# Performance work log

Hardware: AMD Instinct MI355X
Metric: run time of the kernel (lower is better)

Reference implementation:

```python
import jax, jax.numpy as jnp
import numpy as np

EPS = 1e-5
N_HEADS = 16
TOP_K = 2


def _ln(x, g, b):
    m = x.mean(-1, keepdims=True)
    v = ((x - m) ** 2).mean(-1, keepdims=True)
    return (x - m) / jnp.sqrt(v + EPS) * g + b


def _block_fwd(x, ln1_g, ln1_b, ln2_g, ln2_b, Wq, bq, Wk, bk, Wv, bv, Wo, bo,
               Wr, br, e_w1, e_b1, e_w2, e_b2):
    B, S, D = x.shape
    H = N_HEADS
    hd = D // H
    # --- LN + causal MHA + residual (dropout is identity at eval) ---
    h = _ln(x, ln1_g, ln1_b)
    q = (h @ Wq + bq).reshape(B, S, H, hd).transpose(0, 2, 1, 3)  # [B,H,S,hd]
    k = (h @ Wk + bk).reshape(B, S, H, hd).transpose(0, 2, 1, 3)
    v = (h @ Wv + bv).reshape(B, S, H, hd).transpose(0, 2, 1, 3)
    scores = jnp.einsum('bhqd,bhkd->bhqk', q, k) / (hd ** 0.5)
    causal = jnp.tril(jnp.ones((S, S), dtype=bool))
    scores = jnp.where(causal, scores, -jnp.inf)
    attn = jax.nn.softmax(scores, axis=-1)
    o = jnp.einsum('bhqk,bhkd->bhqd', attn, v).transpose(0, 2, 1, 3).reshape(B, S, D)
    a = (o @ Wo + bo) + x
    # --- LN + dense-computed SparseMoE + residual ---
    h2 = _ln(a, ln2_g, ln2_b)
    logits = h2 @ Wr + br                         # [B,S,E]
    topv = jax.lax.top_k(logits, TOP_K)[0]        # [B,S,K]
    kmask = logits >= topv[..., -1:]
    w = jax.nn.softmax(jnp.where(kmask, logits, -jnp.inf), axis=-1)  # [B,S,E]
    # dense per-expert FFN, exactly as the torch module computes it
    mid = jax.nn.gelu(jnp.einsum('bsd,edf->bsef', h2, e_w1) + e_b1,
                      approximate=False)          # [B,S,E,4D]
    eo = jnp.einsum('bsef,efd->bsed', mid, e_w2) + e_b2  # [B,S,E,D]
    moe = jnp.einsum('bse,bsed->bsd', w, eo)
    return moe + a


def setup_inputs() -> dict:
    key = jax.random.key(0)
    B, S, D, E = 1, 2048, 1024, 8
    F = 4 * D
    ks = jax.random.split(key, 8)

    def n(k, shape):
        return jax.random.normal(k, shape, jnp.float32) * 0.02

    return dict(
        x=jax.random.normal(ks[0], (B, S, D), jnp.float32),
        ln1_g=jnp.ones((D,), jnp.float32), ln1_b=jnp.zeros((D,), jnp.float32),
        ln2_g=jnp.ones((D,), jnp.float32), ln2_b=jnp.zeros((D,), jnp.float32),
        Wq=n(ks[1], (D, D)), bq=jnp.zeros((D,), jnp.float32),
        Wk=n(ks[2], (D, D)), bk=jnp.zeros((D,), jnp.float32),
        Wv=n(ks[3], (D, D)), bv=jnp.zeros((D,), jnp.float32),
        Wo=n(ks[4], (D, D)), bo=jnp.zeros((D,), jnp.float32),
        Wr=n(ks[5], (D, E)), br=jnp.zeros((E,), jnp.float32),
        e_w1=n(ks[6], (E, D, F)), e_b1=jnp.zeros((E, F), jnp.float32),
        e_w2=n(ks[7], (E, F, D)), e_b2=jnp.zeros((E, D), jnp.float32),
    )


def reference(x, ln1_g, ln1_b, ln2_g, ln2_b, Wq, bq, Wk, bk, Wv, bv, Wo, bo,
              Wr, br, e_w1, e_b1, e_w2, e_b2):
    return _block_fwd(x, ln1_g, ln1_b, ln2_g, ln2_b, Wq, bq, Wk, bk, Wv, bv,
                      Wo, bo, Wr, br, e_w1, e_b1, e_w2, e_b2)
```

## Files before the change

kernel.cpp:

```cpp
#include <hip/hip_runtime.h>
#include <hip/hip_bf16.h>
#include <math.h>

#define S 2048
#define Dm 1024
#define Ee 8
#define Ff 4096

typedef __attribute__((ext_vector_type(8))) short bf16x8;
typedef __attribute__((ext_vector_type(4))) float f32x4;

__device__ __forceinline__ unsigned short f2bf(float f) {
    union { float f; unsigned int u; } c; c.f = f;
    unsigned int r = (c.u + 0x7fffu + ((c.u >> 16) & 1u)) >> 16;
    return (unsigned short)r;
}

__device__ __forceinline__ void gload16(const void* g, void* l) {
    __builtin_amdgcn_global_load_lds(
        (const __attribute__((address_space(1))) void*)g,
        (__attribute__((address_space(3))) void*)l, 16, 0, 0);
}

__device__ __forceinline__ float gelu_f(float x) {
    float ax = fabsf(x) * 0.70710678118654752f;
    float t = 1.0f / (1.0f + 0.3275911f * ax);
    float p = t * (0.254829592f + t * (-0.284496736f + t * (1.421413741f +
              t * (-1.453152027f + t * 1.061405429f))));
    float er = 1.0f - p * __expf(-ax * ax);
    er = (x < 0.0f) ? -er : er;
    return 0.5f * x * (1.0f + er);
}

__global__ __launch_bounds__(256) void ln_kernel(const float* __restrict__ x,
                                                 const float* __restrict__ g,
                                                 const float* __restrict__ b,
                                                 unsigned short* __restrict__ obf) {
    int row = blockIdx.x;
    int tid = threadIdx.x;
    float4 v = ((const float4*)(x + (size_t)row * Dm))[tid];
    float s  = v.x + v.y + v.z + v.w;
    float sq = v.x*v.x + v.y*v.y + v.z*v.z + v.w*v.w;
    #pragma unroll
    for (int off = 1; off < 64; off <<= 1) {
        s  += __shfl_xor(s, off);
        sq += __shfl_xor(sq, off);
    }
    __shared__ float ps[4], pq[4];
    int wave = tid >> 6;
    if ((tid & 63) == 0) { ps[wave] = s; pq[wave] = sq; }
    __syncthreads();
    s  = ps[0] + ps[1] + ps[2] + ps[3];
    sq = pq[0] + pq[1] + pq[2] + pq[3];
    float mean = s * (1.0f / Dm);
    float var  = sq * (1.0f / Dm) - mean * mean;
    float rstd = rsqrtf(var + 1e-5f);
    float4 gv = ((const float4*)g)[tid];
    float4 bv = ((const float4*)b)[tid];
    float4 o;
    o.x = (v.x - mean) * rstd * gv.x + bv.x;
    o.y = (v.y - mean) * rstd * gv.y + bv.y;
    o.z = (v.z - mean) * rstd * gv.z + bv.z;
    o.w = (v.w - mean) * rstd * gv.w + bv.w;
    unsigned short t4[4] = { f2bf(o.x), f2bf(o.y), f2bf(o.z), f2bf(o.w) };
    *(uint2*)(obf + (size_t)row * Dm + tid * 4) = *(uint2*)t4;
}

__global__ __launch_bounds__(256) void ln2_fused(const float* __restrict__ x,
                                                 const float* __restrict__ p0,
                                                 const float* __restrict__ p1,
                                                 const float* __restrict__ bo,
                                                 const float* __restrict__ g,
                                                 const float* __restrict__ b,
                                                 const float* __restrict__ Wr,
                                                 const float* __restrict__ br,
                                                 float* __restrict__ aout,
                                                 unsigned short* __restrict__ h2b,
                                                 float* __restrict__ w_rt) {
    int row = blockIdx.x;
    int tid = threadIdx.x;
    size_t base = (size_t)row * Dm;
    float4 xv = ((const float4*)(x + base))[tid];
    float4 a0 = ((const float4*)(p0 + base))[tid];
    float4 a1 = ((const float4*)(p1 + base))[tid];
    float4 bv0 = ((const float4*)bo)[tid];
    float4 a;
    a.x = xv.x + a0.x + a1.x + bv0.x;
    a.y = xv.y + a0.y + a1.y + bv0.y;
    a.z = xv.z + a0.z + a1.z + bv0.z;
    a.w = xv.w + a0.w + a1.w + bv0.w;
    ((float4*)(aout + base))[tid] = a;
    float s  = a.x + a.y + a.z + a.w;
    float sq = a.x*a.x + a.y*a.y + a.z*a.z + a.w*a.w;
    #pragma unroll
    for (int off = 1; off < 64; off <<= 1) {
        s  += __shfl_xor(s, off);
        sq += __shfl_xor(sq, off);
    }
    __shared__ float ps[4], pq[4];
    int wave = tid >> 6;
    if ((tid & 63) == 0) { ps[wave] = s; pq[wave] = sq; }
    __syncthreads();
    s  = ps[0] + ps[1] + ps[2] + ps[3];
    sq = pq[0] + pq[1] + pq[2] + pq[3];
    float mean = s * (1.0f / Dm);
    float var  = sq * (1.0f / Dm) - mean * mean;
    float rstd = rsqrtf(var + 1e-5f);
    float4 gv = ((const float4*)g)[tid];
    float4 bbv = ((const float4*)b)[tid];
    float4 o;
    o.x = (a.x - mean) * rstd * gv.x + bbv.x;
    o.y = (a.y - mean) * rstd * gv.y + bbv.y;
    o.z = (a.z - mean) * rstd * gv.z + bbv.z;
    o.w = (a.w - mean) * rstd * gv.w + bbv.w;
    unsigned short t4[4] = { f2bf(o.x), f2bf(o.y), f2bf(o.z), f2bf(o.w) };
    *(uint2*)(h2b + base + tid * 4) = *(uint2*)t4;

    float lg[8];
    #pragma unroll
    for (int e = 0; e < 8; e++) lg[e] = 0.0f;
    float oc[4] = { o.x, o.y, o.z, o.w };
    #pragma unroll
    for (int c = 0; c < 4; c++) {
        const float4* wr4 = (const float4*)(Wr + (size_t)(tid * 4 + c) * Ee);
        float4 wa = wr4[0], wb = wr4[1];
        lg[0] += oc[c]*wa.x; lg[1] += oc[c]*wa.y; lg[2] += oc[c]*wa.z; lg[3] += oc[c]*wa.w;
        lg[4] += oc[c]*wb.x; lg[5] += oc[c]*wb.y; lg[6] += oc[c]*wb.z; lg[7] += oc[c]*wb.w;
    }
    #pragma unroll
    for (int e = 0; e < 8; e++)
        #pragma unroll
        for (int off = 1; off < 64; off <<= 1) lg[e] += __shfl_xor(lg[e], off);
    __shared__ float wlg[4][8];
    if ((tid & 63) == 0) {
        #pragma unroll
        for (int e = 0; e < 8; e++) wlg[wave][e] = lg[e];
    }
    __syncthreads();
    if (tid == 0) {
        float l8[8];
        #pragma unroll
        for (int e = 0; e < 8; e++) l8[e] = wlg[0][e] + wlg[1][e] + wlg[2][e] + wlg[3][e] + br[e];
        float v1 = -INFINITY, v2 = -INFINITY;
        for (int e = 0; e < 8; e++) {
            float xv2 = l8[e];
            if (xv2 > v1) { v2 = v1; v1 = xv2; }
            else if (xv2 > v2) v2 = xv2;
        }
        float wv[8]; float denom = 0.0f;
        for (int e = 0; e < 8; e++) {
            if (l8[e] >= v2) { wv[e] = __expf(l8[e] - v1); denom += wv[e]; }
            else wv[e] = 0.0f;
        }
        float inv = 1.0f / denom;
        for (int e = 0; e < 8; e++) w_rt[row * Ee + e] = wv[e] * inv;
    }
}

__global__ __launch_bounds__(256) void tconv(const float* __restrict__ src,
                                             unsigned short* __restrict__ dst,
                                             int Kk, int Nn) {
    src += (size_t)blockIdx.z * Kk * Nn;
    dst += (size_t)blockIdx.z * Kk * Nn;
    int n0 = blockIdx.x * 64, k0 = blockIdx.y * 64;
    int tid = threadIdx.x;
    __shared__ float t[64][65];
    #pragma unroll
    for (int p = 0; p < 4; p++) {
        int kr = p * 16 + (tid >> 4);
        int nc = (tid & 15) * 4;
        float4 v = *(const float4*)(src + (size_t)(k0 + kr) * Nn + n0 + nc);
        t[kr][nc] = v.x; t[kr][nc+1] = v.y; t[kr][nc+2] = v.z; t[kr][nc+3] = v.w;
    }
    __syncthreads();
    int nr = tid >> 2;
    int kc = (tid & 3) * 16;
    unsigned short o[16];
    #pragma unroll
    for (int j = 0; j < 16; j++) o[j] = f2bf(t[kc + j][nr]);
    *(bf16x8*)(dst + (size_t)(n0 + nr) * Kk + k0 + kc)     = *(bf16x8*)&o[0];
    *(bf16x8*)(dst + (size_t)(n0 + nr) * Kk + k0 + kc + 8) = *(bf16x8*)&o[8];
}

template<int MODE>
__global__ __launch_bounds__(256, 2) void gemm_db(const unsigned short* __restrict__ A,
                                                  const unsigned short* __restrict__ Wt,
                                                  const float* __restrict__ bias0,
                                                  const float* __restrict__ bias1,
                                                  const float* __restrict__ bias2,
                                                  void* __restrict__ Cout,
                                                  int M, int N, int K) {
    const int tid = threadIdx.x;
    const int lane = tid & 63;
    const int w = tid >> 6;
    const int lr = lane >> 4, lc = lane & 15;
    const int wr = w >> 1, wc = w & 1;

    int kc = (MODE == 1) ? blockIdx.z : 0;
    const int m0 = blockIdx.y * 128;
    const int n0 = blockIdx.x * 128;
    const int KL   = (MODE == 1) ? 512 : K;
    const int Koff = kc * KL;

    __shared__ __align__(16) unsigned short As[2][128 * 64];
    __shared__ __align__(16) unsigned short Bs[2][128 * 64];

    const int srow = lane >> 3;
    const int csw  = ((lane & 7) ^ srow) * 8;
    const unsigned short* asrc[4];
    const unsigned short* bsrc[4];
    #pragma unroll
    for (int i = 0; i < 4; i++) {
        int rl = w * 32 + i * 8 + srow;
        asrc[i] = A  + (size_t)(m0 + rl) * K + Koff + csw;
        bsrc[i] = Wt + (size_t)(n0 + rl) * K + Koff + csw;
    }

    f32x4 acc[4][4];
    #pragma unroll
    for (int a = 0; a < 4; a++)
        #pragma unroll
        for (int bb = 0; bb < 4; bb++) acc[a][bb] = (f32x4)0.0f;

    auto STAGE = [&](int buf, int kblk) {
        const size_t koff = (size_t)kblk * 64;
        #pragma unroll
        for (int i = 0; i < 4; i++) {
            gload16(asrc[i] + koff, &As[buf][(w * 32 + i * 8) * 64]);
            gload16(bsrc[i] + koff, &Bs[buf][(w * 32 + i * 8) * 64]);
        }
    };

    const int nt = KL / 64;
    STAGE(0, 0);
    for (int t = 0; t < nt; ++t) {
        const int cur = t & 1;
        if (t + 1 < nt) {
            STAGE(cur ^ 1, t + 1);
            asm volatile("s_waitcnt vmcnt(8)" ::: "memory");
        } else {
            asm volatile("s_waitcnt vmcnt(0)" ::: "memory");
        }
        __builtin_amdgcn_s_barrier();
        #pragma unroll
        for (int ks = 0; ks < 2; ks++) {
            const int ck = ((ks * 4 + lr) ^ (lc & 7)) * 8;
            bf16x8 af[4], bfv[4];
            #pragma unroll
            for (int fm = 0; fm < 4; fm++)
                af[fm] = *(const bf16x8*)&As[cur][(wr * 64 + fm * 16 + lc) * 64 + ck];
            #pragma unroll
            for (int fn = 0; fn < 4; fn++)
                bfv[fn] = *(const bf16x8*)&Bs[cur][(wc * 64 + fn * 16 + lc) * 64 + ck];
            #pragma unroll
            for (int fm = 0; fm < 4; fm++)
                #pragma unroll
                for (int fn = 0; fn < 4; fn++)
                    acc[fm][fn] = __builtin_amdgcn_mfma_f32_16x16x32_bf16(af[fm], bfv[fn], acc[fm][fn], 0, 0, 0);
        }
        asm volatile("" ::: "memory");
        __builtin_amdgcn_s_barrier();
    }

    #pragma unroll
    for (int fm = 0; fm < 4; fm++) {
        #pragma unroll
        for (int r = 0; r < 4; r++) {
            int m = m0 + wr * 64 + fm * 16 + lr * 4 + r;
            #pragma unroll
            for (int fn = 0; fn < 4; fn++) {
                int ncol = n0 + wc * 64 + fn * 16 + lc;
                float val = acc[fm][fn][r];
                if constexpr (MODE == 0) {
                    const float* bb = (ncol < 1024) ? bias0 : (ncol < 2048 ? bias1 : bias2);
                    val += bb[ncol & 1023];
                    ((unsigned short*)Cout)[(size_t)m * N + ncol] = f2bf(val);
                } else {
                    ((float*)Cout)[(size_t)kc * M * N + (size_t)m * N + ncol] = val;
                }
            }
        }
    }
}

template<int MODE>
__global__ __launch_bounds__(256, 2) void gemm_fat(const unsigned short* __restrict__ A,
                                                   const unsigned short* __restrict__ Wt,
                                                   const float* __restrict__ bias,
                                                   void* __restrict__ Cout,
                                                   const int* __restrict__ rows,
                                                   const int* __restrict__ counts,
                                                   const int* __restrict__ offs,
                                                   int N, int K) {
    const int tid = threadIdx.x;
    const int lane = tid & 63;
    const int w = tid >> 6;
    const int lr = lane >> 4, lc = lane & 15;
    const int wm = w >> 1, wn = w & 1;

    int e, kc;
    if constexpr (MODE == 2) { e = blockIdx.z; kc = 0; }
    else { e = blockIdx.z >> 2; kc = blockIdx.z & 3; }
    const int Mcnt = counts[e];
    const int m0 = blockIdx.y * 256;
    if (m0 >= Mcnt) return;
    const int n0 = blockIdx.x * 128;
    const int KL = (MODE == 3) ? (K >> 2) : K;
    const int Koff = kc * KL;
    const unsigned short* Wz = Wt + (size_t)e * N * K;
    const float* biasz = bias + (size_t)e * N;
    const int zoff = offs[e];

    __shared__ __align__(16) unsigned short As[256 * 64];
    __shared__ __align__(16) unsigned short Bs[128 * 64];

    const int srow = lane >> 3;
    const int csw  = ((lane & 7) ^ srow) * 8;
    const unsigned short* asrc[8];
    const unsigned short* bsrc[4];
    #pragma unroll
    for (int i = 0; i < 8; i++) {
        int rl = w * 64 + i * 8 + srow;
        int ma = m0 + rl;
        int srcRow;
        if constexpr (MODE == 2) srcRow = rows[e * S + (ma < Mcnt ? ma : Mcnt - 1)];
        else                     srcRow = zoff + (ma < Mcnt ? ma : Mcnt - 1);
        asrc[i] = A + (size_t)srcRow * K + Koff + csw;
    }
    #pragma unroll
    for (int i = 0; i < 4; i++) {
        int rl = w * 32 + i * 8 + srow;
        bsrc[i] = Wz + (size_t)(n0 + rl) * K + Koff + csw;
    }

    int aBase[2], bBase[2];
    #pragma unroll
    for (int ks = 0; ks < 2; ks++) {
        int ck = ((ks * 4 + lr) ^ (lc & 7)) * 8;
        aBase[ks] = (wm * 128 + lc) * 64 + ck;
        bBase[ks] = (wn * 64  + lc) * 64 + ck;
    }

    f32x4 acc[8][4];
    #pragma unroll
    for (int a = 0; a < 8; a++)
        #pragma unroll
        for (int bb = 0; bb < 4; bb++) acc[a][bb] = (f32x4)0.0f;

    const int nt = KL / 64;
    for (int t = 0; t < nt; ++t) {
        const size_t koff = (size_t)t * 64;
        #pragma unroll
        for (int i = 0; i < 8; i++) gload16(asrc[i] + koff, &As[(w * 64 + i * 8) * 64]);
        #pragma unroll
        for (int i = 0; i < 4; i++) gload16(bsrc[i] + koff, &Bs[(w * 32 + i * 8) * 64]);
        __syncthreads();
        #pragma unroll
        for (int ks = 0; ks < 2; ks++) {
            bf16x8 af[8], bfv[4];
            #pragma unroll
            for (int fm = 0; fm < 8; fm++)
                af[fm] = *(const bf16x8*)&As[aBase[ks] + fm * 1024];
            #pragma unroll
            for (int fn = 0; fn < 4; fn++)
                bfv[fn] = *(const bf16x8*)&Bs[bBase[ks] + fn * 1024];
            #pragma unroll
            for (int fm = 0; fm < 8; fm++)
                #pragma unroll
                for (int fn = 0; fn < 4; fn++)
                    acc[fm][fn] = __builtin_amdgcn_mfma_f32_16x16x32_bf16(af[fm], bfv[fn], acc[fm][fn], 0, 0, 0);
        }
        __syncthreads();
    }

    #pragma unroll
    for (int fm = 0; fm < 8; fm++) {
        #pragma unroll
        for (int r = 0; r < 4; r++) {
            int m = m0 + wm * 128 + fm * 16 + lr * 4 + r;
            if (m >= Mcnt) continue;
            #pragma unroll
            for (int fn = 0; fn < 4; fn++) {
                int ncol = n0 + wn * 64 + fn * 16 + lc;
                float val = acc[fm][fn][r];
                if constexpr (MODE == 2) {
                    val += biasz[ncol];
                    ((unsigned short*)Cout)[(size_t)(zoff + m) * N + ncol] = f2bf(gelu_f(val));
                } else {
                    if (kc == 0) val += biasz[ncol];
                    ((float*)Cout)[(size_t)kc * 4096 * N + (size_t)(zoff + m) * N + ncol] = val;
                }
            }
        }
    }
}

__global__ __launch_bounds__(256) void attn_mfma(const unsigned short* __restrict__ qkv,
                                                 unsigned short* __restrict__ ob) {
    int qt = (int)gridDim.x - 1 - (int)blockIdx.x;
    int h  = blockIdx.y;
    int tid = threadIdx.x;
    int lane = tid & 63, w = tid >> 6;
    int lr = lane >> 4, lc = lane & 15;

    __shared__ __align__(16) unsigned short Kl[2][64 * 64];
    __shared__ __align__(16) unsigned short Vt[2][64 * 64];
    __shared__ __align__(16) unsigned short Pl[4][16 * 64];

    bf16x8 qf[2];
    int qg_base = qt * 64 + w * 16;
    {
        int qrow = qg_base + lc;
        #pragma unroll
        for (int ks = 0; ks < 2; ks++)
            qf[ks] = *(const bf16x8*)(qkv + (size_t)qrow * 3072 + h * 64 + ks * 32 + lr * 8);
    }

    const int srow = lane >> 3;
    const int scw  = ((lane & 7) ^ srow) * 8;
    const unsigned short* ksrc[2];
    #pragma unroll
    for (int i = 0; i < 2; i++)
        ksrc[i] = qkv + (size_t)(w * 16 + i * 8 + srow) * 3072 + h * 64 + 1024 + scw;
    int vrow[2], vcg[2];
    const unsigned short* vsrc[2];
    #pragma unroll
    for (int i = 0; i < 2; i++) {
        int u = tid + i * 256;
        vrow[i] = u >> 3; vcg[i] = (u & 7) * 8;
        vsrc[i] = qkv + (size_t)vrow[i] * 3072 + h * 64 + 2048 + vcg[i];
    }

    f32x4 oacc[4];
    #pragma unroll
    for (int fd = 0; fd < 4; fd++) oacc[fd] = (f32x4)0.0f;
    float mrun[4], lrun[4];
    #pragma unroll
    for (int r = 0; r < 4; r++) { mrun[r] = -INFINITY; lrun[r] = 0.0f; }

    bf16x8 vreg[2];
    vreg[0] = *(const bf16x8*)(vsrc[0]);
    vreg[1] = *(const bf16x8*)(vsrc[1]);
    gload16(ksrc[0], &Kl[0][(w * 16 + 0) * 64]);
    gload16(ksrc[1], &Kl[0][(w * 16 + 8) * 64]);
    #pragma unroll
    for (int i = 0; i < 2; i++)
        #pragma unroll
        for (int j = 0; j < 8; j++) {
            int d = vcg[i] + j;
            int ch = ((vrow[i] >> 3) ^ (d & 7) ^ (d >> 3)) & 7;
            Vt[0][d * 64 + ch * 8 + (vrow[i] & 7)] = (unsigned short)vreg[i][j];
        }
    __syncthreads();

    for (int kt = 0; kt <= qt; kt++) {
        const int cur = kt & 1;
        if (kt < qt) {
            size_t off = (size_t)(kt + 1) * 64 * 3072;
            vreg[0] = *(const bf16x8*)(vsrc[0] + off);
            vreg[1] = *(const bf16x8*)(vsrc[1] + off);
            gload16(ksrc[0] + off, &Kl[cur ^ 1][(w * 16 + 0) * 64]);
            gload16(ksrc[1] + off, &Kl[cur ^ 1][(w * 16 + 8) * 64]);
        }

        f32x4 sc[4];
        #pragma unroll
        for (int fn = 0; fn < 4; fn++) sc[fn] = (f32x4)0.0f;
        #pragma unroll
        for (int fn = 0; fn < 4; fn++)
            #pragma unroll
            for (int ks = 0; ks < 2; ks++) {
                bf16x8 kf = *(const bf16x8*)&Kl[cur][(fn * 16 + lc) * 64 + ((ks * 4 + lr) ^ (lc & 7)) * 8];
                sc[fn] = __builtin_amdgcn_mfma_f32_16x16x32_bf16(qf[ks], kf, sc[fn], 0, 0, 0);
            }

        float st[4][4];
        float mloc[4];
        #pragma unroll
        for (int r = 0; r < 4; r++) mloc[r] = -INFINITY;
        #pragma unroll
        for (int fn = 0; fn < 4; fn++)
            #pragma unroll
            for (int r = 0; r < 4; r++) {
                float sv = sc[fn][r] * 0.125f;
                if (kt == qt) {
                    int kvg = kt * 64 + fn * 16 + lc;
                    int qg  = qg_base + lr * 4 + r;
                    if (kvg > qg) sv = -INFINITY;
                }
                st[fn][r] = sv;
                mloc[r] = fmaxf(mloc[r], sv);
            }
        #pragma unroll
        for (int r = 0; r < 4; r++) {
            mloc[r] = fmaxf(mloc[r], __shfl_xor(mloc[r], 1));
            mloc[r] = fmaxf(mloc[r], __shfl_xor(mloc[r], 2));
            mloc[r] = fmaxf(mloc[r], __shfl_xor(mloc[r], 4));
            mloc[r] = fmaxf(mloc[r], __shfl_xor(mloc[r], 8));
        }
        float fsc[4], lpart[4];
        #pragma unroll
        for (int r = 0; r < 4; r++) {
            float mnew = fmaxf(mrun[r], mloc[r]);
            fsc[r] = __expf(mrun[r] - mnew);
            mrun[r] = mnew;
            lpart[r] = 0.0f;
        }
        float pv[4][4];
        #pragma unroll
        for (int fn = 0; fn < 4; fn++)
            #pragma unroll
            for (int r = 0; r < 4; r++) {
                pv[fn][r] = __expf(st[fn][r] - mrun[r]);
                lpart[r] += pv[fn][r];
            }
        #pragma unroll
        for (int r = 0; r < 4; r++) {
            lpart[r] += __shfl_xor(lpart[r], 1);
            lpart[r] += __shfl_xor(lpart[r], 2);
            lpart[r] += __shfl_xor(lpart[r], 4);
            lpart[r] += __shfl_xor(lpart[r], 8);
            lrun[r] = lrun[r] * fsc[r] + lpart[r];
        }
        #pragma unroll
        for (int fn = 0; fn < 4; fn++)
            #pragma unroll
            for (int r = 0; r < 4; r++) {
                int q = lr * 4 + r;
                int kvc = fn * 16 + lc;
                int ch = ((kvc >> 3) ^ (q & 7) ^ (q >> 3)) & 7;
                Pl[w][q * 64 + ch * 8 + (kvc & 7)] = f2bf(pv[fn][r]);
            }
        #pragma unroll
        for (int fd = 0; fd < 4; fd++)
            #pragma unroll
            for (int r = 0; r < 4; r++) oacc[fd][r] *= fsc[r];

        if (kt < qt) {
            #pragma unroll
            for (int i = 0; i < 2; i++)
                #pragma unroll
                for (int j = 0; j < 8; j++) {
                    int d = vcg[i] + j;
                    int ch = ((vrow[i] >> 3) ^ (d & 7) ^ (d >> 3)) & 7;
                    Vt[cur ^ 1][d * 64 + ch * 8 + (vrow[i] & 7)] = (unsigned short)vreg[i][j];
                }
        }

        __syncthreads();

        #pragma unroll
        for (int ks = 0; ks < 2; ks++) {
            int chp = ((ks * 4 + lr) ^ (lc & 7) ^ (lc >> 3)) & 7;
            bf16x8 pa = *(const bf16x8*)&Pl[w][lc * 64 + chp * 8];
            #pragma unroll
            for (int fd = 0; fd < 4; fd++) {
                int d = fd * 16 + lc;
                int chv = ((ks * 4 + lr) ^ (d & 7) ^ (d >> 3)) & 7;
                bf16x8 vb = *(const bf16x8*)&Vt[cur][d * 64 + chv * 8];
                oacc[fd] = __builtin_amdgcn_mfma_f32_16x16x32_bf16(pa, vb, oacc[fd], 0, 0, 0);
            }
        }
        __syncthreads();
    }
    #pragma unroll
    for (int fd = 0; fd < 4; fd++)
        #pragma unroll
        for (int r = 0; r < 4; r++) {
            float val = oacc[fd][r] / lrun[r];
            ob[(size_t)(qg_base + lr * 4 + r) * 1024 + h * 64 + fd * 16 + lc] = f2bf(val);
        }
}

__global__ __launch_bounds__(256) void listbuild_kernel(const float* __restrict__ w_rt,
                                                        int* __restrict__ rows,
                                                        int* __restrict__ counts,
                                                        int* __restrict__ offs,
                                                        int* __restrict__ tok2slot,
                                                        float* __restrict__ tokw) {
    int tid = threadIdx.x;
    __shared__ int sc[256];
    __shared__ int runoff_s;
    int ncnt[8];
    #pragma unroll
    for (int j = 0; j < 8; j++) ncnt[j] = 0;
    if (tid == 0) runoff_s = 0;
    __syncthreads();
    for (int e = 0; e < Ee; e++) {
        int t0 = tid * 8;
        int sel = 0, flags = 0;
        #pragma unroll
        for (int j = 0; j < 8; j++)
            if (w_rt[(size_t)(t0 + j) * Ee + e] > 0.0f) { flags |= 1 << j; sel++; }
        sc[tid] = sel;
        __syncthreads();
        for (int off = 1; off < 256; off <<= 1) {
            int add = (tid >= off) ? sc[tid - off] : 0;
            __syncthreads();
            sc[tid] += add;
            __syncthreads();
        }
        int base = runoff_s;
        int pos = sc[tid] - sel;
        #pragma unroll
        for (int j = 0; j < 8; j++) {
            if (flags & (1 << j)) {
                rows[e * S + pos] = t0 + j;
                int c = ncnt[j];
                if (c < 2) {
                    tok2slot[(t0 + j) * 2 + c] = base + pos;
                    tokw[(t0 + j) * 2 + c] = w_rt[(size_t)(t0 + j) * Ee + e];
                    ncnt[j] = c + 1;
                }
                pos++;
            }
        }
        __syncthreads();
        if (tid == 0) {
            offs[e] = base;
            counts[e] = sc[255];
            runoff_s = base + sc[255];
        }
        __syncthreads();
    }
}

__global__ __launch_bounds__(256) void combine_kernel(float* __restrict__ out,
                                                      const float* __restrict__ eo,
                                                      const int* __restrict__ tok2slot,
                                                      const float* __restrict__ tokw) {
    int t = blockIdx.x, d = threadIdx.x;
    int s0 = tok2slot[t * 2], s1 = tok2slot[t * 2 + 1];
    float w0 = tokw[t * 2], w1 = tokw[t * 2 + 1];
    float4 o = ((const float4*)(out + (size_t)t * Dm))[d];
    float ax = 0, ay = 0, az = 0, aw = 0, bx = 0, by = 0, bz = 0, bw = 0;
    #pragma unroll
    for (int p = 0; p < 4; p++) {
        const float* ep = eo + (size_t)p * 4096 * Dm;
        float4 a = ((const float4*)(ep + (size_t)s0 * Dm))[d];
        float4 b = ((const float4*)(ep + (size_t)s1 * Dm))[d];
        ax += a.x; ay += a.y; az += a.z; aw += a.w;
        bx += b.x; by += b.y; bz += b.z; bw += b.w;
    }
    o.x += w0 * ax + w1 * bx;
    o.y += w0 * ay + w1 * by;
    o.z += w0 * az + w1 * bz;
    o.w += w0 * aw + w1 * bw;
    ((float4*)(out + (size_t)t * Dm))[d] = o;
}

extern "C" void kernel_launch(void* const* d_in, const int* in_sizes, int n_in,
                              void* d_out, int out_size, void* d_ws, size_t ws_size,
                              hipStream_t stream) {
    const float* x    = (const float*)d_in[0];
    const float* ln1g = (const float*)d_in[1];
    const float* ln1b = (const float*)d_in[2];
    const float* ln2g = (const float*)d_in[3];
    const float* ln2b = (const float*)d_in[4];
    const float* Wq   = (const float*)d_in[5];
    const float* bq   = (const float*)d_in[6];
    const float* Wk   = (const float*)d_in[7];
    const float* bk   = (const float*)d_in[8];
    const float* Wv   = (const float*)d_in[9];
    const float* bv   = (const float*)d_in[10];
    const float* Wo   = (const float*)d_in[11];
    const float* bo   = (const float*)d_in[12];
    const float* Wr   = (const float*)d_in[13];
    const float* br   = (const float*)d_in[14];
    const float* ew1  = (const float*)d_in[15];
    const float* eb1  = (const float*)d_in[16];
    const float* ew2  = (const float*)d_in[17];
    const float* eb2  = (const float*)d_in[18];
    float* out = (float*)d_out;

    char* wsb = (char*)d_ws;
    const size_t MB = 1 << 20;
    unsigned short* ew1T = (unsigned short*)(wsb);
    float*          eo   = (float*)         (wsb);
    unsigned short* ew2T = (unsigned short*)(wsb + 64*MB);
    unsigned short* mid  = (unsigned short*)(wsb + 128*MB);
    unsigned short* qkvT = (unsigned short*)(wsb + 160*MB);
    unsigned short* WoT  = (unsigned short*)(wsb + 166*MB);
    unsigned short* h_bf = (unsigned short*)(wsb + 168*MB);
    unsigned short* qkv  = (unsigned short*)(wsb + 172*MB);
    float*          p01  = (float*)         (wsb + 168*MB);
    unsigned short* ob   = (unsigned short*)(wsb + 184*MB);
    unsigned short* h2b  = (unsigned short*)(wsb + 196*MB);
    float*          w_rt = (float*)         (wsb + 200*MB);
    int*            rows = (int*)           (wsb + 200*MB + 65536);
    int*            counts   = rows + Ee * S;
    int*            offs     = counts + Ee;
    int*            tok2slot = offs + Ee;
    float*          tokw     = (float*)(tok2slot + 2 * S);

    tconv<<<dim3(16, 16, 1), 256, 0, stream>>>(Wq, qkvT,               Dm, Dm);
    tconv<<<dim3(16, 16, 1), 256, 0, stream>>>(Wk, qkvT + 1024*1024,   Dm, Dm);
    tconv<<<dim3(16, 16, 1), 256, 0, stream>>>(Wv, qkvT + 2*1024*1024, Dm, Dm);
    tconv<<<dim3(16, 16, 1), 256, 0, stream>>>(Wo, WoT,                Dm, Dm);
    tconv<<<dim3(64, 16, 8), 256, 0, stream>>>(ew1, ew1T, Dm, Ff);
    tconv<<<dim3(16, 64, 8), 256, 0, stream>>>(ew2, ew2T, Ff, Dm);

    ln_kernel<<<S, 256, 0, stream>>>(x, ln1g, ln1b, h_bf);

    gemm_db<0><<<dim3(24, 16), 256, 0, stream>>>(h_bf, qkvT, bq, bk, bv,
        qkv, S, 3072, Dm);

    attn_mfma<<<dim3(32, 16), 256, 0, stream>>>(qkv, ob);

    gemm_db<1><<<dim3(8, 16, 2), 256, 0, stream>>>(ob, WoT, nullptr, nullptr, nullptr,
        p01, S, Dm, Dm);

    ln2_fused<<<S, 256, 0, stream>>>(x, p01, p01 + (size_t)S * Dm, bo, ln2g, ln2b,
                                     Wr, br, out, h2b, w_rt);
    listbuild_kernel<<<1, 256, 0, stream>>>(w_rt, rows, counts, offs, tok2slot, tokw);

    gemm_fat<2><<<dim3(32, 8, 8), 256, 0, stream>>>(h2b, ew1T, eb1,
        mid, rows, counts, offs, Ff, Dm);

    gemm_fat<3><<<dim3(8, 8, 32), 256, 0, stream>>>(mid, ew2T, eb2,
        eo, rows, counts, offs, Dm, Ff);

    combine_kernel<<<S, 256, 0, stream>>>(out, eo, tok2slot, tokw);
}
```

Measured before the change: 430.7 us.

## Double-buffer MoE expert GEMM with 8-wave blocks, XCD remap, split-K halved

Rewrites the expert FFN GEMM to use 512 threads (8 waves, each with a 64x64 sub-tile) and double-buffered LDS, so the next K-tile is prefetched via global_load_lds while the current one feeds MFMAs, with explicit vmcnt waits. Block indices are remapped so consecutive tiles land on the same XCD for L2 locality. The second GEMM's split-K goes from 4 to 2 partitions, and the combine kernel now reduces only 2 partials. LDS doubles to 96KB per block, which limits occupancy, and the hand-written waitcnt/barrier sync risks subtle races.

```diff
diff --git a/kernel.cpp b/kernel.cpp
--- a/kernel.cpp
+++ b/kernel.cpp
@@ -284,7 +284,7 @@
 }
 
 template<int MODE>
-__global__ __launch_bounds__(256, 2) void gemm_fat(const unsigned short* __restrict__ A,
+__global__ __launch_bounds__(512, 2) void gemm_fat(const unsigned short* __restrict__ A,
                                                    const unsigned short* __restrict__ Wt,
                                                    const float* __restrict__ bias,
                                                    void* __restrict__ Cout,
@@ -298,29 +298,41 @@
     const int lr = lane >> 4, lc = lane & 15;
     const int wm = w >> 1, wn = w & 1;
 
+    const int nx = gridDim.x, ny = gridDim.y;
+    const int nwg = nx * ny * gridDim.z;
+    int b = (int)blockIdx.x + nx * ((int)blockIdx.y + ny * (int)blockIdx.z);
+    {
+        int q = nwg >> 3, r = nwg & 7;
+        int xcd = b & 7, idx = b >> 3;
+        b = ((xcd < r) ? xcd * (q + 1) : r * (q + 1) + (xcd - r) * q) + idx;
+    }
+    const int by = b % ny;
+    const int bx = (b / ny) % nx;
+    const int bz = b / (ny * nx);
+
     int e, kc;
-    if constexpr (MODE == 2) { e = blockIdx.z; kc = 0; }
-    else { e = blockIdx.z >> 2; kc = blockIdx.z & 3; }
+    if constexpr (MODE == 2) { e = bz; kc = 0; }
+    else { e = bz >> 1; kc = bz & 1; }
     const int Mcnt = counts[e];
-    const int m0 = blockIdx.y * 256;
+    const int m0 = by * 256;
     if (m0 >= Mcnt) return;
-    const int n0 = blockIdx.x * 128;
-    const int KL = (MODE == 3) ? (K >> 2) : K;
+    const int n0 = bx * 128;
+    const int KL = (MODE == 3) ? (K >> 1) : K;
     const int Koff = kc * KL;
     const unsigned short* Wz = Wt + (size_t)e * N * K;
     const float* biasz = bias + (size_t)e * N;
     const int zoff = offs[e];
 
-    __shared__ __align__(16) unsigned short As[256 * 64];
-    __shared__ __align__(16) unsigned short Bs[128 * 64];
+    __shared__ __align__(16) unsigned short As[2][256 * 64];
+    __shared__ __align__(16) unsigned short Bs[2][128 * 64];
 
     const int srow = lane >> 3;
     const int csw  = ((lane & 7) ^ srow) * 8;
-    const unsigned short* asrc[8];
-    const unsigned short* bsrc[4];
-    #pragma unroll
-    for (int i = 0; i < 8; i++) {
-        int rl = w * 64 + i * 8 + srow;
+    const unsigned short* asrc[4];
+    const unsigned short* bsrc[2];
+    #pragma unroll
+    for (int i = 0; i < 4; i++) {
+        int rl = i * 64 + w * 8 + srow;
         int ma = m0 + rl;
         int srcRow;
         if constexpr (MODE == 2) srcRow = rows[e * S + (ma < Mcnt ? ma : Mcnt - 1)];
@@ -328,56 +340,63 @@
         asrc[i] = A + (size_t)srcRow * K + Koff + csw;
     }
     #pragma unroll
-    for (int i = 0; i < 4; i++) {
-        int rl = w * 32 + i * 8 + srow;
+    for (int i = 0; i < 2; i++) {
+        int rl = i * 64 + w * 8 + srow;
         bsrc[i] = Wz + (size_t)(n0 + rl) * K + Koff + csw;
     }
 
-    int aBase[2], bBase[2];
-    #pragma unroll
-    for (int ks = 0; ks < 2; ks++) {
-        int ck = ((ks * 4 + lr) ^ (lc & 7)) * 8;
-        aBase[ks] = (wm * 128 + lc) * 64 + ck;
-        bBase[ks] = (wn * 64  + lc) * 64 + ck;
-    }
-
-    f32x4 acc[8][4];
-    #pragma unroll
-    for (int a = 0; a < 8; a++)
+    f32x4 acc[4][4];
+    #pragma unroll
+    for (int a = 0; a < 4; a++)
         #pragma unroll
         for (int bb = 0; bb < 4; bb++) acc[a][bb] = (f32x4)0.0f;
 
+    auto STAGE = [&](int buf, int kblk) {
+        const size_t koff = (size_t)kblk * 64;
+        #pragma unroll
+        for (int i = 0; i < 4; i++)
+            gload16(asrc[i] + koff, &As[buf][(i * 64 + w * 8) * 64]);
+        #pragma unroll
+        for (int i = 0; i < 2; i++)
+            gload16(bsrc[i] + koff, &Bs[buf][(i * 64 + w * 8) * 64]);
+    };
+
     const int nt = KL / 64;
+    STAGE(0, 0);
     for (int t = 0; t < nt; ++t) {
-        const size_t koff = (size_t)t * 64;
-        #pragma unroll
-        for (int i = 0; i < 8; i++) gload16(asrc[i] + koff, &As[(w * 64 + i * 8) * 64]);
-        #pragma unroll
-        for (int i = 0; i < 4; i++) gload16(bsrc[i] + koff, &Bs[(w * 32 + i * 8) * 64]);
-        __syncthreads();
+        const int cur = t & 1;
+        if (t + 1 < nt) {
+            STAGE(cur ^ 1, t + 1);
+            asm volatile("s_waitcnt vmcnt(6)" ::: "memory");
+        } else {
+            asm volatile("s_waitcnt vmcnt(0)" ::: "memory");
+        }
+        __builtin_amdgcn_s_barrier();
         #pragma unroll
         for (int ks = 0; ks < 2; ks++) {
-            bf16x8 af[8], bfv[4];
-            #pragma unroll
-            for (int fm = 0; fm < 8; fm++)
-                af[fm] = *(const bf16x8*)&As[aBase[ks] + fm * 1024];
+            const int ck = ((ks * 4 + lr) ^ (lc & 7)) * 8;
+            bf16x8 af[4], bfv[4];
+            #pragma unroll
+            for (int fm = 0; fm < 4; fm++)
+                af[fm] = *(const bf16x8*)&As[cur][(wm * 64 + fm * 16 + lc) * 64 + ck];
             #pragma unroll
             for (int fn = 0; fn < 4; fn++)
-                bfv[fn] = *(const bf16x8*)&Bs[bBase[ks] + fn * 1024];
-            #pragma unroll
-            for (int fm = 0; fm < 8; fm++)
+                bfv[fn] = *(const bf16x8*)&Bs[cur][(wn * 64 + fn * 16 + lc) * 64 + ck];
+            #pragma unroll
+            for (int fm = 0; fm < 4; fm++)
                 #pragma unroll
                 for (int fn = 0; fn < 4; fn++)
                     acc[fm][fn] = __builtin_amdgcn_mfma_f32_16x16x32_bf16(af[fm], bfv[fn], acc[fm][fn], 0, 0, 0);
         }
-        __syncthreads();
-    }
-
-    #pragma unroll
-    for (int fm = 0; fm < 8; fm++) {
+        asm volatile("" ::: "memory");
+        __builtin_amdgcn_s_barrier();
+    }
+
+    #pragma unroll
+    for (int fm = 0; fm < 4; fm++) {
         #pragma unroll
         for (int r = 0; r < 4; r++) {
-            int m = m0 + wm * 128 + fm * 16 + lr * 4 + r;
+            int m = m0 + wm * 64 + fm * 16 + lr * 4 + r;
             if (m >= Mcnt) continue;
             #pragma unroll
             for (int fn = 0; fn < 4; fn++) {
@@ -635,7 +654,7 @@
     float4 o = ((const float4*)(out + (size_t)t * Dm))[d];
     float ax = 0, ay = 0, az = 0, aw = 0, bx = 0, by = 0, bz = 0, bw = 0;
     #pragma unroll
-    for (int p = 0; p < 4; p++) {
+    for (int p = 0; p < 2; p++) {
         const float* ep = eo + (size_t)p * 4096 * Dm;
         float4 a = ((const float4*)(ep + (size_t)s0 * Dm))[d];
         float4 b = ((const float4*)(ep + (size_t)s1 * Dm))[d];
@@ -714,10 +733,10 @@
                                      Wr, br, out, h2b, w_rt);
     listbuild_kernel<<<1, 256, 0, stream>>>(w_rt, rows, counts, offs, tok2slot, tokw);
 
-    gemm_fat<2><<<dim3(32, 8, 8), 256, 0, stream>>>(h2b, ew1T, eb1,
+    gemm_fat<2><<<dim3(32, 8, 8), 512, 0, stream>>>(h2b, ew1T, eb1,
         mid, rows, counts, offs, Ff, Dm);
 
-    gemm_fat<3><<<dim3(8, 8, 32), 256, 0, stream>>>(mid, ew2T, eb2,
+    gemm_fat<3><<<dim3(8, 8, 16), 512, 0, stream>>>(mid, ew2T, eb2,
         eo, rows, counts, offs, Dm, Ff);
 
     combine_kernel<<<S, 256, 0, stream>>>(out, eo, tok2slot, tokw);
```

Measured after the change: 493.1 us. +14.5%, slower.
